# Kernel tuning notes

Measured on AMD Instinct MI355X. Metric: run time of the kernel, lower is better.

Reference implementation:

```python
import jax, jax.numpy as jnp
import numpy as np

N, E = 50000, 800000
IN_F, C, H, OUT_F = 128, 32, 4, 4
HC = H * C
EPS = 1e-5


def gatv2(x, src, dst, ea, Wl, Wr, We, att, bias, concat):
    # x: [N, in], ea: [E, 1], Wl/Wr: [in, H*C], We: [1, H*C], att: [h, C]
    h, c = att.shape
    xl = (x @ Wl).reshape(-1, h, c)          # [N, h, c]
    xr = (x @ Wr).reshape(-1, h, c)          # [N, h, c]
    m = xl[src] + xr[dst] + (ea @ We).reshape(-1, h, c)   # [E, h, c]
    e = jnp.einsum('ehc,hc->eh', jax.nn.leaky_relu(m, 0.2), att)  # [E, h]
    emax = jax.ops.segment_max(e, dst, num_segments=N)
    e = jnp.exp(e - emax[dst])
    denom = jax.ops.segment_sum(e, dst, num_segments=N)
    alpha = e / (denom[dst] + 1e-16)         # [E, h]
    out = jax.ops.segment_sum(alpha[:, :, None] * xl[src], dst, num_segments=N)  # [N, h, c]
    out = out.reshape(N, h * c) if concat else out.mean(axis=1)
    return out + bias


def bn_eval(x, g, b, m, v):
    return (x - m) * jax.lax.rsqrt(v + EPS) * g + b


def setup_inputs() -> dict:
    key = jax.random.key(0)
    ks = iter(jax.random.split(key, 40))
    nrm = lambda shape, s=0.2: jax.random.normal(next(ks), shape, jnp.float32) * s
    d = {}
    d['x'] = jax.random.normal(next(ks), (N, IN_F), jnp.float32)
    d['edge_index'] = jax.random.randint(next(ks), (2, E), 0, N, jnp.int32)
    d['edge_attr'] = jax.random.normal(next(ks), (E, 1), jnp.float32)
    # layer 1
    d['l1_Wl'] = nrm((IN_F, HC)); d['l1_Wr'] = nrm((IN_F, HC))
    d['l1_We'] = nrm((1, HC)); d['l1_att'] = nrm((H, C)); d['l1_b'] = nrm((HC,))
    # layers 2-9 stacked
    d['mid_Wl'] = nrm((8, HC, HC)); d['mid_Wr'] = nrm((8, HC, HC))
    d['mid_We'] = nrm((8, 1, HC)); d['mid_att'] = nrm((8, H, C)); d['mid_b'] = nrm((8, HC))
    # layer 10: heads=1, concat=False
    d['l10_Wl'] = nrm((HC, C)); d['l10_Wr'] = nrm((HC, C))
    d['l10_We'] = nrm((1, C)); d['l10_att'] = nrm((1, C)); d['l10_b'] = nrm((C,))
    # batchnorms (eval mode): bn1-9 stacked, bn10 separate
    d['bn_g'] = jax.random.uniform(next(ks), (9, HC), jnp.float32, 0.5, 1.5)
    d['bn_b'] = nrm((9, HC)); d['bn_m'] = nrm((9, HC))
    d['bn_v'] = jax.random.uniform(next(ks), (9, HC), jnp.float32, 0.5, 1.5)
    d['bn10_g'] = jax.random.uniform(next(ks), (C,), jnp.float32, 0.5, 1.5)
    d['bn10_b'] = nrm((C,)); d['bn10_m'] = nrm((C,))
    d['bn10_v'] = jax.random.uniform(next(ks), (C,), jnp.float32, 0.5, 1.5)
    d['lin_W'] = nrm((C, OUT_F)); d['lin_b'] = nrm((OUT_F,))
    return d


def reference(x, edge_index, edge_attr,
              l1_Wl, l1_Wr, l1_We, l1_att, l1_b,
              mid_Wl, mid_Wr, mid_We, mid_att, mid_b,
              l10_Wl, l10_Wr, l10_We, l10_att, l10_b,
              bn_g, bn_b, bn_m, bn_v,
              bn10_g, bn10_b, bn10_m, bn10_v,
              lin_W, lin_b):
    src, dst = edge_index[0], edge_index[1]
    h = jax.nn.relu(gatv2(x, src, dst, edge_attr, l1_Wl, l1_Wr, l1_We, l1_att, l1_b, True))
    h = bn_eval(h, bn_g[0], bn_b[0], bn_m[0], bn_v[0])
    for i in range(8):  # layers 2-9
        h = jax.nn.relu(gatv2(h, src, dst, edge_attr, mid_Wl[i], mid_Wr[i], mid_We[i], mid_att[i], mid_b[i], True))
        h = bn_eval(h, bn_g[i + 1], bn_b[i + 1], bn_m[i + 1], bn_v[i + 1])
    h = jax.nn.relu(gatv2(h, src, dst, edge_attr, l10_Wl, l10_Wr, l10_We, l10_att, l10_b, False))
    h = bn_eval(h, bn10_g, bn10_b, bn10_m, bn10_v)
    return h @ lin_W + lin_b
```

## Files before the change

### kernel.cpp

```cpp
#include <hip/hip_runtime.h>
#include <math.h>

#define NN 50000
#define EE 800000
#define EPS 1e-5f
#define SCAN_CH 196

#define NEG_BIG (-1e30f)
#define RESCALE_THR 4.0f

#define LO_SCALE 2048.0f
#define LO_INV   (1.0f/2048.0f)

typedef unsigned short u16;
typedef _Float16 f16x8 __attribute__((ext_vector_type(8)));
typedef float f32x4 __attribute__((ext_vector_type(4)));

__device__ __forceinline__ u16 f2h(float f) {
    _Float16 h = (_Float16)f;
    return __builtin_bit_cast(u16, h);
}
__device__ __forceinline__ float h2f(u16 u) {
    return (float)__builtin_bit_cast(_Float16, u);
}

__device__ __forceinline__ float dpp_add8(float x) {
    int t;
    t = __builtin_amdgcn_update_dpp(0, __float_as_int(x), 0xB1, 0xf, 0xf, true);
    x += __int_as_float(t);
    t = __builtin_amdgcn_update_dpp(0, __float_as_int(x), 0x4E, 0xf, 0xf, true);
    x += __int_as_float(t);
    t = __builtin_amdgcn_update_dpp(0, __float_as_int(x), 0x141, 0xf, 0xf, true);
    x += __int_as_float(t);
    return x;
}

__global__ void hist_kernel(const int* __restrict__ dst, int* cnt) {
    int e = blockIdx.x * blockDim.x + threadIdx.x;
    if (e < EE) atomicAdd(&cnt[dst[e]], 1);
}

__global__ void scan_part(const int* __restrict__ cnt, int* __restrict__ part) {
    __shared__ int red[256];
    int b = blockIdx.x, t = threadIdx.x;
    int i = b * SCAN_CH + t;
    int v = (t < SCAN_CH && i < NN) ? cnt[i] : 0;
    red[t] = v;
    __syncthreads();
#pragma unroll
    for (int s = 128; s; s >>= 1) {
        if (t < s) red[t] += red[t + s];
        __syncthreads();
    }
    if (t == 0) part[b] = red[0];
}

__global__ void scan_block(int* part) {
    __shared__ int buf[2][256];
    int t = threadIdx.x;
    int v = part[t];
    int p = 0;
    buf[0][t] = v;
    __syncthreads();
#pragma unroll
    for (int off = 1; off < 256; off <<= 1) {
        buf[p ^ 1][t] = buf[p][t] + ((t >= off) ? buf[p][t - off] : 0);
        __syncthreads();
        p ^= 1;
    }
    part[t] = buf[p][t] - v;
}

__global__ void scan_final(int* __restrict__ cntcur, const int* __restrict__ part,
                           int* __restrict__ row_start) {
    __shared__ int buf[2][256];
    int b = blockIdx.x, t = threadIdx.x;
    int i = b * SCAN_CH + t;
    int v = (t < SCAN_CH && i < NN) ? cntcur[i] : 0;
    int p = 0;
    buf[0][t] = v;
    __syncthreads();
#pragma unroll
    for (int off = 1; off < 256; off <<= 1) {
        buf[p ^ 1][t] = buf[p][t] + ((t >= off) ? buf[p][t - off] : 0);
        __syncthreads();
        p ^= 1;
    }
    if (t < SCAN_CH && i < NN) {
        int pos = part[b] + buf[p][t] - v;
        row_start[i] = pos;
        cntcur[i] = pos;
    }
    if (b == 0 && t == 0) row_start[NN] = EE;
}

__global__ void scatter_kernel(const int* __restrict__ ei, const float* __restrict__ ea,
                               int* cursor, int2* __restrict__ edge_pack) {
    int e = blockIdx.x * blockDim.x + threadIdx.x;
    if (e < EE) {
        int d = ei[EE + e];
        int pos = atomicAdd(&cursor[d], 1);
        edge_pack[pos] = make_int2(ei[e], __float_as_int(ea[e]));
    }
}

__global__ void split_f32(const float* __restrict__ in, u16* __restrict__ hi,
                          u16* __restrict__ lo, int n4) {
    int i = blockIdx.x * blockDim.x + threadIdx.x;
    if (i >= n4) return;
    float4 v = ((const float4*)in)[i];
    ushort4 h, l;
    h.x = f2h(v.x); l.x = f2h((v.x - h2f(h.x)) * LO_SCALE);
    h.y = f2h(v.y); l.y = f2h((v.y - h2f(h.y)) * LO_SCALE);
    h.z = f2h(v.z); l.z = f2h((v.z - h2f(h.z)) * LO_SCALE);
    h.w = f2h(v.w); l.w = f2h((v.w - h2f(h.w)) * LO_SCALE);
    ((ushort4*)hi)[i] = h;
    ((ushort4*)lo)[i] = l;
}

__global__ void conv_w(const float* __restrict__ l1Wl, const float* __restrict__ l1Wr,
                       const float* __restrict__ midWl, const float* __restrict__ midWr,
                       u16* __restrict__ Wh, u16* __restrict__ Wlo) {
    int tid = blockIdx.x * 256 + threadIdx.x;
    if (tid >= 9 * 256 * 128) return;
    int L = tid >> 15;
    int rem = tid & 32767;
    int n = rem >> 7, k = rem & 127;
    const float* WL;
    const float* WR;
    if (L == 0) { WL = l1Wl; WR = l1Wr; }
    else {
        WL = midWl + (size_t)(L - 1) * 16384;
        WR = midWr + (size_t)(L - 1) * 16384;
    }
    float w = (n < 128) ? WL[k * 128 + n] : WR[k * 128 + (n - 128)];
    u16 h = f2h(w);
    Wh[tid] = h;
    Wlo[tid] = f2h((w - h2f(h)) * LO_SCALE);
}

__global__ __launch_bounds__(256) void gemm_mfma(const u16* __restrict__ Ah,
                                                 const u16* __restrict__ Al,
                                                 const u16* __restrict__ Bh,
                                                 const u16* __restrict__ Bl,
                                                 float* __restrict__ C) {
    int w    = threadIdx.x >> 6;
    int lane = threadIdx.x & 63;
    int lr = lane & 15;
    int kg = lane >> 4;
    int rowbase = blockIdx.x * 64;
    int colb = w * 32;
    int colbase = blockIdx.y * 128 + colb;

    f16x8 bh[2][4], bl[2][4];
#pragma unroll
    for (int ct = 0; ct < 2; ++ct) {
        size_t boff = (size_t)(colbase + ct * 16 + lr) * 128 + (size_t)(kg * 8);
#pragma unroll
        for (int ks = 0; ks < 4; ++ks) {
            bh[ct][ks] = *(const f16x8*)(Bh + boff + ks * 32);
            bl[ct][ks] = *(const f16x8*)(Bl + boff + ks * 32);
        }
    }

    auto aoff_of = [&](int rt) {
        int arow = rowbase + rt * 16 + lr;
        if (arow >= NN) arow = NN - 1;
        return (size_t)arow * 128 + (size_t)(kg * 8);
    };
    f16x8 ahc[4], alc[4], ahn[4], aln[4];
    {
        size_t ao = aoff_of(0);
#pragma unroll
        for (int ks = 0; ks < 4; ++ks) {
            ahc[ks] = *(const f16x8*)(Ah + ao + ks * 32);
            alc[ks] = *(const f16x8*)(Al + ao + ks * 32);
        }
    }

    float* Cp = C + (size_t)blockIdx.y * ((size_t)NN * 128);

#pragma unroll
    for (int rt = 0; rt < 4; ++rt) {
        if (rt < 3) {
            size_t ao = aoff_of(rt + 1);
#pragma unroll
            for (int ks = 0; ks < 4; ++ks) {
                ahn[ks] = *(const f16x8*)(Ah + ao + ks * 32);
                aln[ks] = *(const f16x8*)(Al + ao + ks * 32);
            }
        }

        f32x4 aH[2], aL[2];
#pragma unroll
        for (int ct = 0; ct < 2; ++ct) {
            aH[ct] = (f32x4){0.f, 0.f, 0.f, 0.f};
            aL[ct] = (f32x4){0.f, 0.f, 0.f, 0.f};
        }
#pragma unroll
        for (int ks = 0; ks < 4; ++ks) {
#pragma unroll
            for (int ct = 0; ct < 2; ++ct) {
                aH[ct] = __builtin_amdgcn_mfma_f32_16x16x32_f16(ahc[ks], bh[ct][ks], aH[ct], 0, 0, 0);
                aL[ct] = __builtin_amdgcn_mfma_f32_16x16x32_f16(alc[ks], bh[ct][ks], aL[ct], 0, 0, 0);
                aL[ct] = __builtin_amdgcn_mfma_f32_16x16x32_f16(ahc[ks], bl[ct][ks], aL[ct], 0, 0, 0);
            }
        }

        int crow0 = rowbase + rt * 16 + kg * 4;
#pragma unroll
        for (int ct = 0; ct < 2; ++ct) {
            float* cp = Cp + (size_t)crow0 * 128 + colb + ct * 16 + lr;
#pragma unroll
            for (int r = 0; r < 4; ++r) {
                if (crow0 + r < NN)
                    cp[(size_t)r * 128] = fmaf(aL[ct][r], LO_INV, aH[ct][r]);
            }
        }

        if (rt < 3) {
#pragma unroll
            for (int ks = 0; ks < 4; ++ks) { ahc[ks] = ahn[ks]; alc[ks] = aln[ks]; }
        }
    }
}

__global__ __launch_bounds__(256) void gemm_tile(const u16* __restrict__ Ah,
                                                 const u16* __restrict__ Al,
                                                 const float* __restrict__ B,
                                                 float* __restrict__ C,
                                                 int M, int nc, int ldb, int ldc, int coff) {
    __shared__ float As[128][64];
    __shared__ float Bs[128][64];
    int t  = threadIdx.x;
    int bm = blockIdx.x * 64;
    int bn = blockIdx.y * 64;
    {
        int k4 = (t & 31) << 2;
        int r0 = t >> 5;
#pragma unroll
        for (int pass = 0; pass < 8; ++pass) {
            int row = r0 + pass * 8;
            int gm  = bm + row;
            float4 v = make_float4(0.f, 0.f, 0.f, 0.f);
            if (gm < M) {
                ushort4 h = *(const ushort4*)(Ah + (size_t)gm * 128 + k4);
                ushort4 l = *(const ushort4*)(Al + (size_t)gm * 128 + k4);
                v.x = fmaf(h2f(l.x), LO_INV, h2f(h.x));
                v.y = fmaf(h2f(l.y), LO_INV, h2f(h.y));
                v.z = fmaf(h2f(l.z), LO_INV, h2f(h.z));
                v.w = fmaf(h2f(l.w), LO_INV, h2f(h.w));
            }
            As[k4 + 0][row] = v.x; As[k4 + 1][row] = v.y;
            As[k4 + 2][row] = v.z; As[k4 + 3][row] = v.w;
        }
    }
    {
        int c4 = (t & 15) << 2;
        int kr = t >> 4;
#pragma unroll
        for (int pass = 0; pass < 8; ++pass) {
            int k  = kr + pass * 16;
            int gc = bn + c4;
            float4 v = make_float4(0.f, 0.f, 0.f, 0.f);
            if (gc < nc) v = *(const float4*)(B + (size_t)k * ldb + gc);
            *(float4*)&Bs[k][c4] = v;
        }
    }
    __syncthreads();

    int tx = t & 15, ty = t >> 4;
    int m0 = ty * 4, c0 = tx * 4;
    float acc[4][4] = {{0.f}};
#pragma unroll 8
    for (int k = 0; k < 128; ++k) {
        float4 av = *(const float4*)&As[k][m0];
        float4 bv = *(const float4*)&Bs[k][c0];
        float a4[4] = {av.x, av.y, av.z, av.w};
        float b4[4] = {bv.x, bv.y, bv.z, bv.w};
#pragma unroll
        for (int i = 0; i < 4; ++i)
#pragma unroll
            for (int j = 0; j < 4; ++j) acc[i][j] = fmaf(a4[i], b4[j], acc[i][j]);
    }
#pragma unroll
    for (int i = 0; i < 4; ++i) {
        int gm = bm + m0 + i;
        int gc = bn + c0;
        if (gm < M && gc < nc) {
            *(float4*)(C + (size_t)gm * ldc + coff + gc) =
                make_float4(acc[i][0], acc[i][1], acc[i][2], acc[i][3]);
        }
    }
}

__global__ __launch_bounds__(256) void node_agg_128(const float* __restrict__ xlr,
                                                    const int* __restrict__ row_start,
                                                    const int2* __restrict__ epack,
                                                    const float* __restrict__ We,
                                                    const float* __restrict__ att,
                                                    const float* __restrict__ bias,
                                                    const float* __restrict__ bng,
                                                    const float* __restrict__ bnb,
                                                    const float* __restrict__ bnm,
                                                    const float* __restrict__ bnv,
                                                    u16* __restrict__ ahi,
                                                    u16* __restrict__ alo) {
    int node = (blockIdx.x * blockDim.x + threadIdx.x) >> 6;
    int lane = threadIdx.x & 63;
    if (node >= NN) return;
    int half = lane >> 5;
    int c0   = (lane & 31) << 2;

    const float* xlp = xlr;
    const float* xrp = xlr + (size_t)NN * 128;

    const float L2E = 1.44269504f;
    const float4 xr4 = *(const float4*)(xrp + (size_t)node * 128 + c0);
    const float4 we4 = *(const float4*)(We + c0);
    const float4 at4 = *(const float4*)(att + c0);
    float4 a6, a4;
    a6.x = 0.6f * L2E * at4.x; a4.x = 0.4f * L2E * at4.x;
    a6.y = 0.6f * L2E * at4.y; a4.y = 0.4f * L2E * at4.y;
    a6.z = 0.6f * L2E * at4.z; a4.z = 0.4f * L2E * at4.z;
    a6.w = 0.6f * L2E * at4.w; a4.w = 0.4f * L2E * at4.w;

    int beg = row_start[node], end = row_start[node + 1];
    int lastE = end - 1;

    float mx0 = NEG_BIG, sm0 = 0.f;
    float mx1 = NEG_BIG, sm1 = 0.f;
    float4 ac0 = make_float4(0.f, 0.f, 0.f, 0.f);
    float4 ac1 = make_float4(0.f, 0.f, 0.f, 0.f);

    auto score = [&](float eav, const float4& xv) -> float {
        float m0 = xv.x + fmaf(eav, we4.x, xr4.x);
        float m1 = xv.y + fmaf(eav, we4.y, xr4.y);
        float m2 = xv.z + fmaf(eav, we4.z, xr4.z);
        float m3 = xv.w + fmaf(eav, we4.w, xr4.w);
        float p = fmaf(a6.x, m0, a4.x * fabsf(m0));
        p = fmaf(a6.y, m1, fmaf(a4.y, fabsf(m1), p));
        p = fmaf(a6.z, m2, fmaf(a4.z, fabsf(m2), p));
        p = fmaf(a6.w, m3, fmaf(a4.w, fabsf(m3), p));
        return dpp_add8(p);
    };

    auto upd = [&](float& mx, float& sm, float4& ac, float p, const float4& xv) {
        float d = p - mx;
        if (__ballot(d > RESCALE_THR)) {
            float nm = fmaxf(mx, p);
            float sc = exp2f(mx - nm);
            float w  = exp2f(p - nm);
            sm = fmaf(sm, sc, w);
            ac.x = fmaf(ac.x, sc, w * xv.x);
            ac.y = fmaf(ac.y, sc, w * xv.y);
            ac.z = fmaf(ac.z, sc, w * xv.z);
            ac.w = fmaf(ac.w, sc, w * xv.w);
            mx = nm;
        } else {
            float w = exp2f(d);
            sm += w;
            ac.x = fmaf(w, xv.x, ac.x);
            ac.y = fmaf(w, xv.y, ac.y);
            ac.z = fmaf(w, xv.z, ac.z);
            ac.w = fmaf(w, xv.w, ac.w);
        }
    };

    int j = beg;
    for (; j + 3 < end; j += 4) {
        int2 pkA = epack[j + half];
        int2 pkB = epack[j + 2 + half];
        float4 xA = *(const float4*)(xlp + ((size_t)pkA.x << 7) + c0);
        float4 xB = *(const float4*)(xlp + ((size_t)pkB.x << 7) + c0);
        float pA = score(__int_as_float(pkA.y), xA);
        float pB = score(__int_as_float(pkB.y), xB);
        upd(mx0, sm0, ac0, pA, xA);
        upd(mx1, sm1, ac1, pB, xB);
    }
    if (j < end) {
        int jeA = j + half;       bool dA = jeA > lastE; if (dA) jeA = lastE;
        int jeB = j + 2 + half;   bool dB = jeB > lastE; if (dB) jeB = lastE;
        int2 pkA = epack[jeA];
        int2 pkB = epack[jeB];
        float4 xA = *(const float4*)(xlp + ((size_t)pkA.x << 7) + c0);
        float4 xB = *(const float4*)(xlp + ((size_t)pkB.x << 7) + c0);
        float pA = score(__int_as_float(pkA.y), xA);
        float pB = score(__int_as_float(pkB.y), xB);
        pA = dA ? NEG_BIG : pA;
        pB = dB ? NEG_BIG : pB;
        upd(mx0, sm0, ac0, pA, xA);
        upd(mx1, sm1, ac1, pB, xB);
    }

    float Mx = fmaxf(mx0, mx1);
    float s0 = exp2f(mx0 - Mx), s1 = exp2f(mx1 - Mx);
    float sm = fmaf(sm0, s0, sm1 * s1);
    float4 ac;
    ac.x = fmaf(ac0.x, s0, ac1.x * s1);
    ac.y = fmaf(ac0.y, s0, ac1.y * s1);
    ac.z = fmaf(ac0.z, s0, ac1.z * s1);
    ac.w = fmaf(ac0.w, s0, ac1.w * s1);

    float  Mo  = __shfl_xor(Mx, 32);
    float  smo = __shfl_xor(sm, 32);
    float4 aco;
    aco.x = __shfl_xor(ac.x, 32);
    aco.y = __shfl_xor(ac.y, 32);
    aco.z = __shfl_xor(ac.z, 32);
    aco.w = __shfl_xor(ac.w, 32);
    float Mn = fmaxf(Mx, Mo);
    float ss = exp2f(Mx - Mn), so = exp2f(Mo - Mn);
    sm   = fmaf(sm, ss, smo * so);
    ac.x = fmaf(ac.x, ss, aco.x * so);
    ac.y = fmaf(ac.y, ss, aco.y * so);
    ac.z = fmaf(ac.z, ss, aco.z * so);
    ac.w = fmaf(ac.w, ss, aco.w * so);

    if (half == 0) {
        float inv = 1.f / (sm + 1e-16f);
        const float4 b4  = *(const float4*)(bias + c0);
        const float4 g4  = *(const float4*)(bng + c0);
        const float4 bb4 = *(const float4*)(bnb + c0);
        const float4 m4  = *(const float4*)(bnm + c0);
        const float4 v4  = *(const float4*)(bnv + c0);
        float4 y;
        y.x = fmaxf(fmaf(ac.x, inv, b4.x), 0.f);
        y.y = fmaxf(fmaf(ac.y, inv, b4.y), 0.f);
        y.z = fmaxf(fmaf(ac.z, inv, b4.z), 0.f);
        y.w = fmaxf(fmaf(ac.w, inv, b4.w), 0.f);
        y.x = (y.x - m4.x) * rsqrtf(v4.x + EPS) * g4.x + bb4.x;
        y.y = (y.y - m4.y) * rsqrtf(v4.y + EPS) * g4.y + bb4.y;
        y.z = (y.z - m4.z) * rsqrtf(v4.z + EPS) * g4.z + bb4.z;
        y.w = (y.w - m4.w) * rsqrtf(v4.w + EPS) * g4.w + bb4.w;

        ushort4 hh, ll;
        hh.x = f2h(y.x); ll.x = f2h((y.x - h2f(hh.x)) * LO_SCALE);
        hh.y = f2h(y.y); ll.y = f2h((y.y - h2f(hh.y)) * LO_SCALE);
        hh.z = f2h(y.z); ll.z = f2h((y.z - h2f(hh.z)) * LO_SCALE);
        hh.w = f2h(y.w); ll.w = f2h((y.w - h2f(hh.w)) * LO_SCALE);
        *(ushort4*)(ahi + (size_t)node * 128 + c0) = hh;
        *(ushort4*)(alo + (size_t)node * 128 + c0) = ll;
    }
}

__global__ __launch_bounds__(256) void node_agg_l10(const float* __restrict__ xlr,
                                                    const int* __restrict__ row_start,
                                                    const int2* __restrict__ epack,
                                                    const float* __restrict__ We,
                                                    const float* __restrict__ att,
                                                    const float* __restrict__ bias,
                                                    const float* __restrict__ bng,
                                                    const float* __restrict__ bnb,
                                                    const float* __restrict__ bnm,
                                                    const float* __restrict__ bnv,
                                                    const float* __restrict__ linW,
                                                    const float* __restrict__ linb,
                                                    float* __restrict__ out) {
    int n = (blockIdx.x * blockDim.x + threadIdx.x) >> 5;
    if (n >= NN) return;
    int q    = threadIdx.x & 31;
    int slot = q >> 3;
    int c0   = (q & 7) << 2;

    const float L2E = 1.44269504f;
    const float4 xr = *(const float4*)(xlr + (size_t)n * 64 + 32 + c0);
    const float4 we = *(const float4*)(We + c0);
    const float4 at = *(const float4*)(att + c0);
    float4 a6, a4;
    a6.x = 0.6f * L2E * at.x; a4.x = 0.4f * L2E * at.x;
    a6.y = 0.6f * L2E * at.y; a4.y = 0.4f * L2E * at.y;
    a6.z = 0.6f * L2E * at.z; a4.z = 0.4f * L2E * at.z;
    a6.w = 0.6f * L2E * at.w; a4.w = 0.4f * L2E * at.w;

    int beg = row_start[n], end = row_start[n + 1];
    int lastE = end - 1;

    float mx = NEG_BIG, sm = 0.f;
    float4 ac = make_float4(0.f, 0.f, 0.f, 0.f);

    auto score4 = [&](float eav, const float4& xv) -> float {
        float m0 = xv.x + fmaf(eav, we.x, xr.x);
        float m1 = xv.y + fmaf(eav, we.y, xr.y);
        float m2 = xv.z + fmaf(eav, we.z, xr.z);
        float m3 = xv.w + fmaf(eav, we.w, xr.w);
        float p = fmaf(a6.x, m0, a4.x * fabsf(m0));
        p = fmaf(a6.y, m1, fmaf(a4.y, fabsf(m1), p));
        p = fmaf(a6.z, m2, fmaf(a4.z, fabsf(m2), p));
        p = fmaf(a6.w, m3, fmaf(a4.w, fabsf(m3), p));
        return dpp_add8(p);
    };

    auto upd = [&](float p, const float4& xv) {
        float d = p - mx;
        if (__ballot(d > RESCALE_THR)) {
            float nm = fmaxf(mx, p);
            float sc = exp2f(mx - nm);
            float w  = exp2f(p - nm);
            sm = fmaf(sm, sc, w);
            ac.x = fmaf(ac.x, sc, w * xv.x); ac.y = fmaf(ac.y, sc, w * xv.y);
            ac.z = fmaf(ac.z, sc, w * xv.z); ac.w = fmaf(ac.w, sc, w * xv.w);
            mx = nm;
        } else {
            float w = exp2f(d);
            sm += w;
            ac.x = fmaf(w, xv.x, ac.x); ac.y = fmaf(w, xv.y, ac.y);
            ac.z = fmaf(w, xv.z, ac.z); ac.w = fmaf(w, xv.w, ac.w);
        }
    };

    int nE = end - beg;
    int last4 = beg + (nE & ~3);

    int2 pkn; float4 xvn;
    if (beg < last4) {
        pkn = epack[beg + slot];
        xvn = *(const float4*)(xlr + ((size_t)pkn.x << 6) + c0);
    }
    for (int j = beg; j < last4; ) {
        int2 pk = pkn; float4 xv = xvn;
        j += 4;
        if (j < last4) {
            pkn = epack[j + slot];
            xvn = *(const float4*)(xlr + ((size_t)pkn.x << 6) + c0);
        }
        float p = score4(__int_as_float(pk.y), xv);
        upd(p, xv);
    }
    if (last4 < end) {
        int je = last4 + slot;
        bool dead = je > lastE; if (dead) je = lastE;
        int2 pk = epack[je];
        float4 xv = *(const float4*)(xlr + ((size_t)pk.x << 6) + c0);
        float p = score4(__int_as_float(pk.y), xv);
        p = dead ? NEG_BIG : p;
        upd(p, xv);
    }

#pragma unroll
    for (int off = 8; off <= 16; off <<= 1) {
        float  Mo  = __shfl_xor(mx, off);
        float  smo = __shfl_xor(sm, off);
        float4 aco;
        aco.x = __shfl_xor(ac.x, off); aco.y = __shfl_xor(ac.y, off);
        aco.z = __shfl_xor(ac.z, off); aco.w = __shfl_xor(ac.w, off);
        float Mn = fmaxf(mx, Mo);
        float ss = exp2f(mx - Mn), so = exp2f(Mo - Mn);
        sm = fmaf(sm, ss, smo * so);
        ac.x = fmaf(ac.x, ss, aco.x * so); ac.y = fmaf(ac.y, ss, aco.y * so);
        ac.z = fmaf(ac.z, ss, aco.z * so); ac.w = fmaf(ac.w, ss, aco.w * so);
        mx = Mn;
    }

    float inv = 1.f / (sm + 1e-16f);
    const float4 b4 = *(const float4*)(bias + c0);
    const float4 g4 = *(const float4*)(bng + c0);
    const float4 q4 = *(const float4*)(bnb + c0);
    const float4 m4 = *(const float4*)(bnm + c0);
    const float4 v4 = *(const float4*)(bnv + c0);
    float4 y;
    y.x = fmaxf(fmaf(ac.x, inv, b4.x), 0.f);
    y.y = fmaxf(fmaf(ac.y, inv, b4.y), 0.f);
    y.z = fmaxf(fmaf(ac.z, inv, b4.z), 0.f);
    y.w = fmaxf(fmaf(ac.w, inv, b4.w), 0.f);
    y.x = (y.x - m4.x) * rsqrtf(v4.x + EPS) * g4.x + q4.x;
    y.y = (y.y - m4.y) * rsqrtf(v4.y + EPS) * g4.y + q4.y;
    y.z = (y.z - m4.z) * rsqrtf(v4.z + EPS) * g4.z + q4.z;
    y.w = (y.w - m4.w) * rsqrtf(v4.w + EPS) * g4.w + q4.w;

    const float4 w0 = *(const float4*)(linW + (c0 + 0) * 4);
    const float4 w1 = *(const float4*)(linW + (c0 + 1) * 4);
    const float4 w2 = *(const float4*)(linW + (c0 + 2) * 4);
    const float4 w3 = *(const float4*)(linW + (c0 + 3) * 4);
    float4 t;
    t.x = fmaf(y.x, w0.x, fmaf(y.y, w1.x, fmaf(y.z, w2.x, y.w * w3.x)));
    t.y = fmaf(y.x, w0.y, fmaf(y.y, w1.y, fmaf(y.z, w2.y, y.w * w3.y)));
    t.z = fmaf(y.x, w0.z, fmaf(y.y, w1.z, fmaf(y.z, w2.z, y.w * w3.z)));
    t.w = fmaf(y.x, w0.w, fmaf(y.y, w1.w, fmaf(y.z, w2.w, y.w * w3.w)));
    t.x = dpp_add8(t.x); t.y = dpp_add8(t.y);
    t.z = dpp_add8(t.z); t.w = dpp_add8(t.w);

    if (q == 0) {
        const float4 lb = *(const float4*)linb;
        float4 o;
        o.x = t.x + lb.x; o.y = t.y + lb.y; o.z = t.z + lb.z; o.w = t.w + lb.w;
        *(float4*)(out + (size_t)n * 4) = o;
    }
}

extern "C" void kernel_launch(void* const* d_in, const int* in_sizes, int n_in,
                              void* d_out, int out_size, void* d_ws, size_t ws_size,
                              hipStream_t stream) {
    const float* x      = (const float*)d_in[0];
    const int*   ei     = (const int*)d_in[1];
    const float* ea     = (const float*)d_in[2];
    const float* l1_Wl  = (const float*)d_in[3];
    const float* l1_Wr  = (const float*)d_in[4];
    const float* l1_We  = (const float*)d_in[5];
    const float* l1_att = (const float*)d_in[6];
    const float* l1_b   = (const float*)d_in[7];
    const float* mid_Wl = (const float*)d_in[8];
    const float* mid_Wr = (const float*)d_in[9];
    const float* mid_We = (const float*)d_in[10];
    const float* mid_att= (const float*)d_in[11];
    const float* mid_b  = (const float*)d_in[12];
    const float* l10_Wl = (const float*)d_in[13];
    const float* l10_Wr = (const float*)d_in[14];
    const float* l10_We = (const float*)d_in[15];
    const float* l10_att= (const float*)d_in[16];
    const float* l10_b  = (const float*)d_in[17];
    const float* bn_g   = (const float*)d_in[18];
    const float* bn_b   = (const float*)d_in[19];
    const float* bn_m   = (const float*)d_in[20];
    const float* bn_v   = (const float*)d_in[21];
    const float* bn10_g = (const float*)d_in[22];
    const float* bn10_b = (const float*)d_in[23];
    const float* bn10_m = (const float*)d_in[24];
    const float* bn10_v = (const float*)d_in[25];
    const float* lin_W  = (const float*)d_in[26];
    const float* lin_b  = (const float*)d_in[27];

    char* ws = (char*)d_ws;
    auto take = [&](size_t bytes) { char* p = ws; ws += (bytes + 255) & ~size_t(255); return p; };
    int*   row_start  = (int*)  take(sizeof(int) * (NN + 1));
    int*   cursor     = (int*)  take(sizeof(int) * NN);
    int*   part       = (int*)  take(sizeof(int) * 256);
    int2*  epack      = (int2*) take(sizeof(int2) * EE);
    float* xlr        = (float*)take(sizeof(float) * (size_t)NN * 256);
    u16*   Ahi        = (u16*)  take(sizeof(u16) * (size_t)NN * 128);
    u16*   Alo        = (u16*)  take(sizeof(u16) * (size_t)NN * 128);
    u16*   Wthi       = (u16*)  take(sizeof(u16) * 9 * 256 * 128);
    u16*   Wtlo       = (u16*)  take(sizeof(u16) * 9 * 256 * 128);

    hipMemsetAsync(cursor, 0, sizeof(int) * NN, stream);
    hist_kernel<<<EE / 256, 256, 0, stream>>>(ei + EE, cursor);
    scan_part<<<256, 256, 0, stream>>>(cursor, part);
    scan_block<<<1, 256, 0, stream>>>(part);
    scan_final<<<256, 256, 0, stream>>>(cursor, part, row_start);
    scatter_kernel<<<EE / 256, 256, 0, stream>>>(ei, ea, cursor, epack);

    split_f32<<<(NN * 128 / 4 + 255) / 256, 256, 0, stream>>>(x, Ahi, Alo, NN * 128 / 4);
    conv_w<<<(9 * 256 * 128 + 255) / 256, 256, 0, stream>>>(l1_Wl, l1_Wr, mid_Wl, mid_Wr,
                                                            Wthi, Wtlo);

    const int GBM = (NN + 63) / 64;
    dim3 gmm(GBM, 2);

    gemm_mfma<<<gmm, 256, 0, stream>>>(Ahi, Alo, Wthi, Wtlo, xlr);
    node_agg_128<<<(NN * 64) / 256, 256, 0, stream>>>(
        xlr, row_start, epack, l1_We, l1_att, l1_b,
        bn_g, bn_b, bn_m, bn_v, Ahi, Alo);

    for (int i = 0; i < 8; ++i) {
        gemm_mfma<<<gmm, 256, 0, stream>>>(Ahi, Alo,
                                           Wthi + (size_t)(i + 1) * 32768,
                                           Wtlo + (size_t)(i + 1) * 32768, xlr);
        node_agg_128<<<(NN * 64) / 256, 256, 0, stream>>>(
            xlr, row_start, epack,
            mid_We + (size_t)i * 128, mid_att + (size_t)i * 128, mid_b + (size_t)i * 128,
            bn_g + (size_t)(i + 1) * 128, bn_b + (size_t)(i + 1) * 128,
            bn_m + (size_t)(i + 1) * 128, bn_v + (size_t)(i + 1) * 128,
            Ahi, Alo);
    }

    const int MB = (NN + 63) / 64;
    dim3 g1(MB, 1);
    gemm_tile<<<g1, 256, 0, stream>>>(Ahi, Alo, l10_Wl, xlr, NN, 32, 32, 64, 0);
    gemm_tile<<<g1, 256, 0, stream>>>(Ahi, Alo, l10_Wr, xlr, NN, 32, 32, 64, 32);
    node_agg_l10<<<(NN * 32 + 255) / 256, 256, 0, stream>>>(
        xlr, row_start, epack, l10_We, l10_att, l10_b,
        bn10_g, bn10_b, bn10_m, bn10_v, lin_W, lin_b, (float*)d_out);
}
```

Measured before the change: 1.247 ms.

## Use split-fp16 MFMA for layer-10 GEMM and swizzle mid-layer GEMM block order

The two FP32 LDS-tiled GEMM launches for layer 10 become one MFMA kernel that uses the same hi/lo fp16 split as the other layers. It reads weights pre-converted by a new conv_w10 kernel and writes both the Wl and Wr outputs into a 64-wide xlr buffer. The main gemm_mfma launch changes from a 2D grid to a 1D grid where groups of 8 row-blocks interleave the two column halves, so the shared A tiles stay in cache between them. This adds a small conversion kernel, and some blocks in the padded grid exit early.

```diff
diff --git a/kernel.cpp b/kernel.cpp
--- a/kernel.cpp
+++ b/kernel.cpp
@@ -139,18 +139,35 @@
     Wlo[tid] = f2h((w - h2f(h)) * LO_SCALE);
 }
 
+__global__ void conv_w10(const float* __restrict__ Wl, const float* __restrict__ Wr,
+                         u16* __restrict__ Wh, u16* __restrict__ Wlo) {
+    int tid = blockIdx.x * 256 + threadIdx.x;
+    if (tid >= 64 * 128) return;
+    int n = tid >> 7, k = tid & 127;
+    float w = (n < 32) ? Wl[k * 32 + n] : Wr[k * 32 + (n - 32)];
+    u16 h = f2h(w);
+    Wh[tid] = h;
+    Wlo[tid] = f2h((w - h2f(h)) * LO_SCALE);
+}
+
 __global__ __launch_bounds__(256) void gemm_mfma(const u16* __restrict__ Ah,
                                                  const u16* __restrict__ Al,
                                                  const u16* __restrict__ Bh,
                                                  const u16* __restrict__ Bl,
                                                  float* __restrict__ C) {
+    int bid = blockIdx.x;
+    int jj = bid & 7;
+    int y  = (bid >> 3) & 1;
+    int x  = (bid >> 4) * 8 + jj;
+    if (x >= (NN + 63) / 64) return;
+
     int w    = threadIdx.x >> 6;
     int lane = threadIdx.x & 63;
     int lr = lane & 15;
     int kg = lane >> 4;
-    int rowbase = blockIdx.x * 64;
+    int rowbase = x * 64;
     int colb = w * 32;
-    int colbase = blockIdx.y * 128 + colb;
+    int colbase = y * 128 + colb;
 
     f16x8 bh[2][4], bl[2][4];
 #pragma unroll
@@ -178,7 +195,7 @@
         }
     }
 
-    float* Cp = C + (size_t)blockIdx.y * ((size_t)NN * 128);
+    float* Cp = C + (size_t)y * ((size_t)NN * 128);
 
 #pragma unroll
     for (int rt = 0; rt < 4; ++rt) {
@@ -225,71 +242,74 @@
     }
 }
 
-__global__ __launch_bounds__(256) void gemm_tile(const u16* __restrict__ Ah,
-                                                 const u16* __restrict__ Al,
-                                                 const float* __restrict__ B,
-                                                 float* __restrict__ C,
-                                                 int M, int nc, int ldb, int ldc, int coff) {
-    __shared__ float As[128][64];
-    __shared__ float Bs[128][64];
-    int t  = threadIdx.x;
-    int bm = blockIdx.x * 64;
-    int bn = blockIdx.y * 64;
+__global__ __launch_bounds__(256) void gemm_mfma_l10(const u16* __restrict__ Ah,
+                                                     const u16* __restrict__ Al,
+                                                     const u16* __restrict__ Bh,
+                                                     const u16* __restrict__ Bl,
+                                                     float* __restrict__ C) {
+    int w    = threadIdx.x >> 6;
+    int lane = threadIdx.x & 63;
+    int lr = lane & 15;
+    int kg = lane >> 4;
+    int rowbase = blockIdx.x * 64;
+    int colb = w * 16;
+
+    f16x8 bh[4], bl[4];
     {
-        int k4 = (t & 31) << 2;
-        int r0 = t >> 5;
-#pragma unroll
-        for (int pass = 0; pass < 8; ++pass) {
-            int row = r0 + pass * 8;
-            int gm  = bm + row;
-            float4 v = make_float4(0.f, 0.f, 0.f, 0.f);
-            if (gm < M) {
-                ushort4 h = *(const ushort4*)(Ah + (size_t)gm * 128 + k4);
-                ushort4 l = *(const ushort4*)(Al + (size_t)gm * 128 + k4);
-                v.x = fmaf(h2f(l.x), LO_INV, h2f(h.x));
-                v.y = fmaf(h2f(l.y), LO_INV, h2f(h.y));
-                v.z = fmaf(h2f(l.z), LO_INV, h2f(h.z));
-                v.w = fmaf(h2f(l.w), LO_INV, h2f(h.w));
+        size_t boff = (size_t)(colb + lr) * 128 + (size_t)(kg * 8);
+#pragma unroll
+        for (int ks = 0; ks < 4; ++ks) {
+            bh[ks] = *(const f16x8*)(Bh + boff + ks * 32);
+            bl[ks] = *(const f16x8*)(Bl + boff + ks * 32);
+        }
+    }
+
+    auto aoff_of = [&](int rt) {
+        int arow = rowbase + rt * 16 + lr;
+        if (arow >= NN) arow = NN - 1;
+        return (size_t)arow * 128 + (size_t)(kg * 8);
+    };
+    f16x8 ahc[4], alc[4], ahn[4], aln[4];
+    {
+        size_t ao = aoff_of(0);
+#pragma unroll
+        for (int ks = 0; ks < 4; ++ks) {
+            ahc[ks] = *(const f16x8*)(Ah + ao + ks * 32);
+            alc[ks] = *(const f16x8*)(Al + ao + ks * 32);
+        }
+    }
+
+#pragma unroll
+    for (int rt = 0; rt < 4; ++rt) {
+        if (rt < 3) {
+            size_t ao = aoff_of(rt + 1);
+#pragma unroll
+            for (int ks = 0; ks < 4; ++ks) {
+                ahn[ks] = *(const f16x8*)(Ah + ao + ks * 32);
+                aln[ks] = *(const f16x8*)(Al + ao + ks * 32);
             }
-            As[k4 + 0][row] = v.x; As[k4 + 1][row] = v.y;
-            As[k4 + 2][row] = v.z; As[k4 + 3][row] = v.w;
-        }
-    }
-    {
-        int c4 = (t & 15) << 2;
-        int kr = t >> 4;
-#pragma unroll
-        for (int pass = 0; pass < 8; ++pass) {
-            int k  = kr + pass * 16;
-            int gc = bn + c4;
-            float4 v = make_float4(0.f, 0.f, 0.f, 0.f);
-            if (gc < nc) v = *(const float4*)(B + (size_t)k * ldb + gc);
-            *(float4*)&Bs[k][c4] = v;
-        }
-    }
-    __syncthreads();
-
-    int tx = t & 15, ty = t >> 4;
-    int m0 = ty * 4, c0 = tx * 4;
-    float acc[4][4] = {{0.f}};
-#pragma unroll 8
-    for (int k = 0; k < 128; ++k) {
-        float4 av = *(const float4*)&As[k][m0];
-        float4 bv = *(const float4*)&Bs[k][c0];
-        float a4[4] = {av.x, av.y, av.z, av.w};
-        float b4[4] = {bv.x, bv.y, bv.z, bv.w};
-#pragma unroll
-        for (int i = 0; i < 4; ++i)
-#pragma unroll
-            for (int j = 0; j < 4; ++j) acc[i][j] = fmaf(a4[i], b4[j], acc[i][j]);
-    }
-#pragma unroll
-    for (int i = 0; i < 4; ++i) {
-        int gm = bm + m0 + i;
-        int gc = bn + c0;
-        if (gm < M && gc < nc) {
-            *(float4*)(C + (size_t)gm * ldc + coff + gc) =
-                make_float4(acc[i][0], acc[i][1], acc[i][2], acc[i][3]);
+        }
+
+        f32x4 aH = (f32x4){0.f, 0.f, 0.f, 0.f};
+        f32x4 aL = (f32x4){0.f, 0.f, 0.f, 0.f};
+#pragma unroll
+        for (int ks = 0; ks < 4; ++ks) {
+            aH = __builtin_amdgcn_mfma_f32_16x16x32_f16(ahc[ks], bh[ks], aH, 0, 0, 0);
+            aL = __builtin_amdgcn_mfma_f32_16x16x32_f16(alc[ks], bh[ks], aL, 0, 0, 0);
+            aL = __builtin_amdgcn_mfma_f32_16x16x32_f16(ahc[ks], bl[ks], aL, 0, 0, 0);
+        }
+
+        int crow0 = rowbase + rt * 16 + kg * 4;
+        float* cp = C + (size_t)crow0 * 64 + colb + lr;
+#pragma unroll
+        for (int r = 0; r < 4; ++r) {
+            if (crow0 + r < NN)
+                cp[(size_t)r * 64] = fmaf(aL[r], LO_INV, aH[r]);
+        }
+
+        if (rt < 3) {
+#pragma unroll
+            for (int ks = 0; ks < 4; ++ks) { ahc[ks] = ahn[ks]; alc[ks] = aln[ks]; }
         }
     }
 }
@@ -631,6 +651,8 @@
     u16*   Alo        = (u16*)  take(sizeof(u16) * (size_t)NN * 128);
     u16*   Wthi       = (u16*)  take(sizeof(u16) * 9 * 256 * 128);
     u16*   Wtlo       = (u16*)  take(sizeof(u16) * 9 * 256 * 128);
+    u16*   Wt10hi     = (u16*)  take(sizeof(u16) * 64 * 128);
+    u16*   Wt10lo     = (u16*)  take(sizeof(u16) * 64 * 128);
 
     hipMemsetAsync(cursor, 0, sizeof(int) * NN, stream);
     hist_kernel<<<EE / 256, 256, 0, stream>>>(ei + EE, cursor);
@@ -642,19 +664,20 @@
     split_f32<<<(NN * 128 / 4 + 255) / 256, 256, 0, stream>>>(x, Ahi, Alo, NN * 128 / 4);
     conv_w<<<(9 * 256 * 128 + 255) / 256, 256, 0, stream>>>(l1_Wl, l1_Wr, mid_Wl, mid_Wr,
                                                             Wthi, Wtlo);
+    conv_w10<<<(64 * 128 + 255) / 256, 256, 0, stream>>>(l10_Wl, l10_Wr, Wt10hi, Wt10lo);
 
     const int GBM = (NN + 63) / 64;
-    dim3 gmm(GBM, 2);
-
-    gemm_mfma<<<gmm, 256, 0, stream>>>(Ahi, Alo, Wthi, Wtlo, xlr);
+    const int GSWZ = ((GBM + 7) / 8) * 16;
+
+    gemm_mfma<<<GSWZ, 256, 0, stream>>>(Ahi, Alo, Wthi, Wtlo, xlr);
     node_agg_128<<<(NN * 64) / 256, 256, 0, stream>>>(
         xlr, row_start, epack, l1_We, l1_att, l1_b,
         bn_g, bn_b, bn_m, bn_v, Ahi, Alo);
 
     for (int i = 0; i < 8; ++i) {
-        gemm_mfma<<<gmm, 256, 0, stream>>>(Ahi, Alo,
-                                           Wthi + (size_t)(i + 1) * 32768,
-                                           Wtlo + (size_t)(i + 1) * 32768, xlr);
+        gemm_mfma<<<GSWZ, 256, 0, stream>>>(Ahi, Alo,
+                                            Wthi + (size_t)(i + 1) * 32768,
+                                            Wtlo + (size_t)(i + 1) * 32768, xlr);
         node_agg_128<<<(NN * 64) / 256, 256, 0, stream>>>(
             xlr, row_start, epack,
             mid_We + (size_t)i * 128, mid_att + (size_t)i * 128, mid_b + (size_t)i * 128,
@@ -663,10 +686,7 @@
             Ahi, Alo);
     }
 
-    const int MB = (NN + 63) / 64;
-    dim3 g1(MB, 1);
-    gemm_tile<<<g1, 256, 0, stream>>>(Ahi, Alo, l10_Wl, xlr, NN, 32, 32, 64, 0);
-    gemm_tile<<<g1, 256, 0, stream>>>(Ahi, Alo, l10_Wr, xlr, NN, 32, 32, 64, 32);
+    gemm_mfma_l10<<<GBM, 256, 0, stream>>>(Ahi, Alo, Wt10hi, Wt10lo, xlr);
     node_agg_l10<<<(NN * 32 + 255) / 256, 256, 0, stream>>>(
         xlr, row_start, epack, l10_We, l10_att, l10_b,
         bn10_g, bn10_b, bn10_m, bn10_v, lin_W, lin_b, (float*)d_out);
```

New measurement: 1.212 ms. 1.03x faster.
